# Kernel optimization log

Measured on AMD Instinct MI355X. Metric: run time of the kernel, lower is better.

Reference implementation:

```python
import jax, jax.numpy as jnp
import numpy as np

N_EXPERTS = 8
TOP_K = 2
LB_COEF = 0.01
D_MODEL = 1024
D_FF = 4096


def setup_inputs() -> dict:
    key = jax.random.key(0)
    k_x, k_r, k_w1, k_w2, k_w3 = jax.random.split(key, 5)
    x = jax.random.normal(k_x, (2, 1024, D_MODEL), dtype=jnp.float32)
    # nn.Linear(d_model, n_experts, bias=False).weight has shape (E, d_model)
    router_w = jax.random.normal(k_r, (N_EXPERTS, D_MODEL), dtype=jnp.float32) * 0.02
    # stacked expert weights; stored pre-transposed for x @ W contractions
    w1 = jax.random.normal(k_w1, (N_EXPERTS, D_MODEL, D_FF), dtype=jnp.float32) * 0.02
    w3 = jax.random.normal(k_w3, (N_EXPERTS, D_MODEL, D_FF), dtype=jnp.float32) * 0.02
    w2 = jax.random.normal(k_w2, (N_EXPERTS, D_FF, D_MODEL), dtype=jnp.float32) * 0.02
    return {"x": x, "router_w": router_w, "w1": w1, "w3": w3, "w2": w2}


def reference(x, router_w, w1, w3, w2):
    B, T, C = x.shape
    xf = x.reshape(-1, C)                      # (N, C), N = B*T
    N = xf.shape[0]

    router_logits = xf @ router_w.T            # (N, E)
    top_v, top_i = jax.lax.top_k(router_logits, TOP_K)
    top_p = jax.nn.softmax(top_v, axis=-1)     # (N, K)

    # combine weight per (token, expert): sum of top-k probs routed to expert e
    comb = jnp.zeros((N, N_EXPERTS), dtype=xf.dtype)
    comb = comb.at[jnp.arange(N)[:, None], top_i].add(top_p)  # (N, E)

    # grouped SwiGLU FFN across all experts (dense-equivalent of masked loop;
    # tokens with zero combine weight contribute nothing)
    gate = jax.nn.silu(jnp.einsum("tc,ecf->etf", xf, w1))     # (E, N, F)
    up = jnp.einsum("tc,ecf->etf", xf, w3)                    # (E, N, F)
    expert_out = jnp.einsum("etf,efc->etc", gate * up, w2)    # (E, N, C)
    out = jnp.einsum("etc,te->tc", expert_out, comb)          # (N, C)

    router_probs = jax.nn.softmax(router_logits, axis=-1)
    expert_probs = router_probs.mean(axis=0)                  # (E,)
    aux_loss = LB_COEF * N_EXPERTS * jnp.sum(expert_probs * expert_probs)

    return out.reshape(B, T, C), aux_loss
```

## Files before the change

kernel.cpp:

```cpp
#include <hip/hip_runtime.h>
#include <hip/hip_bf16.h>
#include <hip/hip_fp16.h>

#define NTOK 2048
#define DM   1024
#define DF   4096
#define NE   8
#define NROWS (NTOK * 2)
#define NSPLIT 4
#define KSPL (DF / NSPLIT)
#define FFN1_NG (32 * 16 * 8)

typedef _Float16 f16x8 __attribute__((ext_vector_type(8)));
typedef float    f32x4 __attribute__((ext_vector_type(4)));
typedef unsigned u32x2 __attribute__((ext_vector_type(2)));

__device__ __forceinline__ void gload_lds16(const void* g, void* l) {
    __builtin_amdgcn_global_load_lds(
        (const __attribute__((address_space(1))) void*)g,
        (__attribute__((address_space(3))) void*)l, 16, 0, 0);
}

__device__ __forceinline__ u32x2 pack4(float4 v) {
    _Float16 a = (_Float16)v.x, b = (_Float16)v.y,
             c = (_Float16)v.z, d = (_Float16)v.w;
    unsigned ua = __builtin_bit_cast(unsigned short, a);
    unsigned ub = __builtin_bit_cast(unsigned short, b);
    unsigned uc = __builtin_bit_cast(unsigned short, c);
    unsigned ud = __builtin_bit_cast(unsigned short, d);
    u32x2 r;
    r[0] = ua | (ub << 16);
    r[1] = uc | (ud << 16);
    return r;
}

__global__ void k_init(int* counts, float* probs_sum) {
    int i = threadIdx.x;
    if (i < NE) { counts[i] = 0; probs_sum[i] = 0.f; }
}

__device__ __forceinline__ void transpose_tile(
    float* tile ,
    const float* __restrict__ src, _Float16* __restrict__ dst,
    int K, int N, int k0, int n0, int tid)
{
    int tk = tid >> 4, tn = (tid & 15) << 2;
#pragma unroll
    for (int r = 0; r < 4; r++) {
        float4 v = *(const float4*)(src + (size_t)(k0 + tk + (r << 4)) * N + n0 + tn);
        float* trow = &tile[(tk + (r << 4)) * 65 + tn];
        trow[0] = v.x; trow[1] = v.y; trow[2] = v.z; trow[3] = v.w;
    }
    __syncthreads();
    int on = tid >> 2, ok = (tid & 3) << 4;
    unsigned pk[8];
#pragma unroll
    for (int p2 = 0; p2 < 8; p2++) {
        _Float16 a = (_Float16)tile[(ok + 2 * p2) * 65 + on];
        _Float16 b = (_Float16)tile[(ok + 2 * p2 + 1) * 65 + on];
        pk[p2] = (unsigned)(*(unsigned short*)&a) | ((unsigned)(*(unsigned short*)&b) << 16);
    }
    _Float16* d = dst + (size_t)(n0 + on) * K + k0 + ok;
    *(uint4*)d       = make_uint4(pk[0], pk[1], pk[2], pk[3]);
    *(uint4*)(d + 8) = make_uint4(pk[4], pk[5], pk[6], pk[7]);
}

__global__ __launch_bounds__(256) void k_pre(
    const float* __restrict__ x, const float* __restrict__ rw,
    const float* __restrict__ w1, const float* __restrict__ w3,
    _Float16* __restrict__ WA, _Float16* __restrict__ WB,
    int* counts, float* probs_sum,
    int* pair_exp, int* pair_pos, float* topp)
{
    __shared__ float smem[64 * 65];
    int bid = blockIdx.x;
    int tid = threadIdx.x;

    if (bid >= 128) {
        int t = bid - 128;
        int z = t >> 10, xy = t & 1023;
        int e = z & 7;
        const float* src = ((z < 8) ? w1 : w3) + (size_t)e * DM * DF;
        _Float16* dst = ((z < 8) ? WA : WB) + (size_t)e * DF * DM;
        transpose_tile(smem, src, dst, DM, DF, (xy >> 6) << 6, (xy & 63) << 6, tid);
        return;
    }

    float* lprobs = smem;
    int* lcount = (int*)(smem + 8);
    int* lbase  = (int*)(smem + 16);
    if (tid < NE) { lprobs[tid] = 0.f; lcount[tid] = 0; }
    __syncthreads();

    int l16 = tid & 15;
    int t = bid * 16 + (tid >> 4);

    const float* xt = x + (size_t)t * DM;
    float acc[NE];
#pragma unroll
    for (int e = 0; e < NE; e++) acc[e] = 0.f;

#pragma unroll
    for (int i0 = 0; i0 < DM; i0 += 64) {
        int i = i0 + l16 * 4;
        float4 xv = *(const float4*)(xt + i);
#pragma unroll
        for (int e = 0; e < NE; e++) {
            float4 wv = *(const float4*)(rw + e * DM + i);
            acc[e] = fmaf(xv.x, wv.x, acc[e]);
            acc[e] = fmaf(xv.y, wv.y, acc[e]);
            acc[e] = fmaf(xv.z, wv.z, acc[e]);
            acc[e] = fmaf(xv.w, wv.w, acc[e]);
        }
    }
#pragma unroll
    for (int m = 1; m < 16; m <<= 1)
#pragma unroll
        for (int e = 0; e < NE; e++)
            acc[e] += __shfl_xor(acc[e], m);

    int i0e = 0, i1e = 0, r0 = 0, r1 = 0;
    if (l16 == 0) {
        float mx = acc[0];
#pragma unroll
        for (int e = 1; e < NE; e++) mx = fmaxf(mx, acc[e]);
        float p[NE]; float s = 0.f;
#pragma unroll
        for (int e = 0; e < NE; e++) { p[e] = expf(acc[e] - mx); s += p[e]; }
        float inv = 1.f / s;
#pragma unroll
        for (int e = 0; e < NE; e++) atomicAdd(&lprobs[e], p[e] * inv);

        i0e = 0;
#pragma unroll
        for (int e = 1; e < NE; e++) if (acc[e] > acc[i0e]) i0e = e;
        i1e = (i0e == 0) ? 1 : 0;
#pragma unroll
        for (int e = 0; e < NE; e++) if (e != i0e && acc[e] > acc[i1e]) i1e = e;

        float e1 = expf(acc[i1e] - acc[i0e]);
        float den = 1.f / (1.f + e1);
        topp[t * 2 + 0] = den;
        topp[t * 2 + 1] = e1 * den;
        pair_exp[t * 2 + 0] = i0e;
        pair_exp[t * 2 + 1] = i1e;
        r0 = atomicAdd(&lcount[i0e], 1);
        r1 = atomicAdd(&lcount[i1e], 1);
    }
    __syncthreads();
    if (tid < NE) {
        lbase[tid] = atomicAdd(&counts[tid], lcount[tid]);
        atomicAdd(&probs_sum[tid], lprobs[tid]);
    }
    __syncthreads();
    if (l16 == 0) {
        pair_pos[t * 2 + 0] = lbase[i0e] + r0;
        pair_pos[t * 2 + 1] = lbase[i1e] + r1;
    }
}

__global__ void k_offsets(const int* counts, const float* probs_sum,
                          int* eoff, float* out_aux)
{
    if (threadIdx.x == 0 && blockIdx.x == 0) {
        int off = 0;
        for (int e = 0; e < NE; e++) { eoff[e] = off; off += counts[e]; }
        eoff[NE] = off;
        float aux = 0.f;
        for (int e = 0; e < NE; e++) {
            float ep = probs_sum[e] / (float)NTOK;
            aux += ep * ep;
        }
        out_aux[0] = 0.01f * (float)NE * aux;
    }
}

__global__ __launch_bounds__(256) void k_gather(
    const float* __restrict__ x, const int* __restrict__ pair_exp,
    const int* __restrict__ pair_pos, const int* __restrict__ eoff,
    _Float16* __restrict__ Xg)
{
    int b = blockIdx.x;
    int t = b >> 1, s = b & 1;
    int e = pair_exp[t * 2 + s];
    int row = eoff[e] + pair_pos[t * 2 + s];
    int c = threadIdx.x << 2;
    float4 v = *(const float4*)(x + (size_t)t * DM + c);
    u32x2 o = pack4(v);
    *(u32x2*)(Xg + (size_t)row * DM + c) = o;
}

__global__ __launch_bounds__(256) void k_transpose(
    const float* __restrict__ W, _Float16* __restrict__ Wt, int K, int N)
{
    __shared__ float tile[64 * 65];
    int e = blockIdx.z;
    transpose_tile(tile, W + (size_t)e * K * N, Wt + (size_t)e * N * K,
                   K, N, blockIdx.y << 6, blockIdx.x << 6, threadIdx.x);
}

__global__ __launch_bounds__(256, 2) void k_ffn1(
    const _Float16* __restrict__ A, const _Float16* __restrict__ B1t,
    const _Float16* __restrict__ B3t, _Float16* __restrict__ H,
    const int* __restrict__ counts, const int* __restrict__ eoff,
    const float* __restrict__ w2, _Float16* __restrict__ W2T)
{
    __shared__ __align__(16) unsigned char smem[49152];
    int bid = blockIdx.x;
    int tid = threadIdx.x;

    if (bid >= FFN1_NG) {
        int t = bid - FFN1_NG;
        int e = t >> 10, xy = t & 1023;
        transpose_tile((float*)smem, w2 + (size_t)e * DF * DM,
                       W2T + (size_t)e * DM * DF,
                       DF, DM, (xy >> 4) << 6, (xy & 15) << 6, tid);
        return;
    }

    int e = bid >> 9;
    int m0 = ((bid >> 5) & 15) << 7;
    int n0 = (bid & 31) << 7;
    int cnt = counts[e];
    if (m0 >= cnt) return;
    int rb = eoff[e];

    int lane = tid & 63, w = tid >> 6;
    int wr = (w >> 1) << 6, wc = (w & 1) << 6;
    int l15 = lane & 15, l4 = lane >> 4;

    const _Float16* Ab  = A   + (size_t)(rb + m0) * DM;
    const _Float16* B1b = B1t + ((size_t)e * DF + n0) * DM;
    const _Float16* B3b = B3t + ((size_t)e * DF + n0) * DM;

    int c0 = tid, c1 = tid + 256;
    int r0c = c0 >> 2, s0c = (c0 & 3) ^ ((r0c >> 1) & 3);
    int r1c = c1 >> 2, s1c = (c1 & 3) ^ ((r1c >> 1) & 3);
    size_t g0 = (size_t)r0c * DM + (s0c << 3);
    size_t g1 = (size_t)r1c * DM + (s1c << 3);

    f32x4 accg[4][4], accu[4][4];
#pragma unroll
    for (int i = 0; i < 4; i++)
#pragma unroll
        for (int j = 0; j < 4; j++) {
            accg[i][j] = (f32x4){0.f, 0.f, 0.f, 0.f};
            accu[i][j] = (f32x4){0.f, 0.f, 0.f, 0.f};
        }

    auto STAGE = [&](unsigned char* buf, int k0) {
        gload_lds16(Ab  + g0 + k0, buf + (c0 << 4));
        gload_lds16(Ab  + g1 + k0, buf + (c1 << 4));
        gload_lds16(B1b + g0 + k0, buf + 8192 + (c0 << 4));
        gload_lds16(B1b + g1 + k0, buf + 8192 + (c1 << 4));
        gload_lds16(B3b + g0 + k0, buf + 16384 + (c0 << 4));
        gload_lds16(B3b + g1 + k0, buf + 16384 + (c1 << 4));
    };
    auto COMPUTE = [&](const unsigned char* buf) {
        f16x8 af[4], b1f[4], b3f[4];
#pragma unroll
        for (int i = 0; i < 4; i++) {
            int r = wr + (i << 4) + l15;
            int s = l4 ^ ((r >> 1) & 3);
            af[i] = *(const f16x8*)(buf + (r << 6) + (s << 4));
        }
#pragma unroll
        for (int j = 0; j < 4; j++) {
            int r = wc + (j << 4) + l15;
            int s = l4 ^ ((r >> 1) & 3);
            int o = (r << 6) + (s << 4);
            b1f[j] = *(const f16x8*)(buf + 8192 + o);
            b3f[j] = *(const f16x8*)(buf + 16384 + o);
        }
        __builtin_amdgcn_s_setprio(1);
#pragma unroll
        for (int i = 0; i < 4; i++)
#pragma unroll
            for (int j = 0; j < 4; j++) {
                accg[i][j] = __builtin_amdgcn_mfma_f32_16x16x32_f16(af[i], b1f[j], accg[i][j], 0, 0, 0);
                accu[i][j] = __builtin_amdgcn_mfma_f32_16x16x32_f16(af[i], b3f[j], accu[i][j], 0, 0, 0);
            }
        __builtin_amdgcn_s_setprio(0);
    };

    unsigned char* cur = smem;
    unsigned char* nxt = smem + 24576;

    STAGE(cur, 0);
    for (int k = 32; k < DM; k += 32) {
        STAGE(nxt, k);
        __builtin_amdgcn_sched_barrier(0);
        asm volatile("s_waitcnt vmcnt(6)" ::: "memory");
        __builtin_amdgcn_s_barrier();
        __builtin_amdgcn_sched_barrier(0);
        COMPUTE(cur);
        __builtin_amdgcn_sched_barrier(0);
        __builtin_amdgcn_s_barrier();
        unsigned char* tp = cur; cur = nxt; nxt = tp;
    }
    asm volatile("s_waitcnt vmcnt(0)" ::: "memory");
    __builtin_amdgcn_s_barrier();
    __builtin_amdgcn_sched_barrier(0);
    COMPUTE(cur);

#pragma unroll
    for (int i = 0; i < 4; i++) {
#pragma unroll
        for (int rr = 0; rr < 4; rr++) {
            int m = m0 + wr + (i << 4) + (l4 << 2) + rr;
            if (m < cnt) {
                size_t go = (size_t)(rb + m) * DF + n0 + wc + l15;
#pragma unroll
                for (int j = 0; j < 4; j++) {
                    float g = accg[i][j][rr];
                    float u = accu[i][j][rr];
                    float h = g / (1.f + __expf(-g)) * u;
                    H[go + (size_t)(j << 4)] = (_Float16)h;
                }
            }
        }
    }
}

__global__ __launch_bounds__(256, 3) void k_gemm2(
    const _Float16* __restrict__ A, const _Float16* __restrict__ Bt,
    float* __restrict__ Yp,
    const int* __restrict__ counts, const int* __restrict__ eoff)
{
    __shared__ __align__(16) unsigned char smem[32768];
    int z = blockIdx.z;
    int e = z >> 2, sp = z & 3;
    int cnt = counts[e];
    int m0 = blockIdx.y << 7;
    if (m0 >= cnt) return;
    int n0 = blockIdx.x << 7;
    int rb = eoff[e];

    int tid = threadIdx.x;
    int lane = tid & 63, w = tid >> 6;
    int wr = (w >> 1) << 6, wc = (w & 1) << 6;
    int l15 = lane & 15, l4 = lane >> 4;

    const _Float16* Ab = A + (size_t)(rb + m0) * DF;
    const _Float16* Bb = Bt + ((size_t)e * DM + n0) * DF;

    int c0 = tid, c1 = tid + 256;
    int r0c = c0 >> 2, s0c = (c0 & 3) ^ ((r0c >> 1) & 3);
    int r1c = c1 >> 2, s1c = (c1 & 3) ^ ((r1c >> 1) & 3);
    size_t g0 = (size_t)r0c * DF + (s0c << 3);
    size_t g1 = (size_t)r1c * DF + (s1c << 3);

    f32x4 acc[4][4];
#pragma unroll
    for (int i = 0; i < 4; i++)
#pragma unroll
        for (int j = 0; j < 4; j++) acc[i][j] = (f32x4){0.f, 0.f, 0.f, 0.f};

    auto STAGE = [&](unsigned char* buf, int k0) {
        gload_lds16(Ab + g0 + k0, buf + (c0 << 4));
        gload_lds16(Ab + g1 + k0, buf + (c1 << 4));
        gload_lds16(Bb + g0 + k0, buf + 8192 + (c0 << 4));
        gload_lds16(Bb + g1 + k0, buf + 8192 + (c1 << 4));
    };
    auto COMPUTE = [&](const unsigned char* buf) {
        f16x8 af[4], bfr[4];
#pragma unroll
        for (int i = 0; i < 4; i++) {
            int r = wr + (i << 4) + l15;
            int s = l4 ^ ((r >> 1) & 3);
            af[i] = *(const f16x8*)(buf + (r << 6) + (s << 4));
        }
#pragma unroll
        for (int j = 0; j < 4; j++) {
            int r = wc + (j << 4) + l15;
            int s = l4 ^ ((r >> 1) & 3);
            bfr[j] = *(const f16x8*)(buf + 8192 + (r << 6) + (s << 4));
        }
        __builtin_amdgcn_s_setprio(1);
#pragma unroll
        for (int i = 0; i < 4; i++)
#pragma unroll
            for (int j = 0; j < 4; j++)
                acc[i][j] = __builtin_amdgcn_mfma_f32_16x16x32_f16(af[i], bfr[j], acc[i][j], 0, 0, 0);
        __builtin_amdgcn_s_setprio(0);
    };

    unsigned char* cur = smem;
    unsigned char* nxt = smem + 16384;
    int kbase = sp * KSPL;

    STAGE(cur, kbase);
    for (int k = 32; k < KSPL; k += 32) {
        STAGE(nxt, kbase + k);
        __builtin_amdgcn_sched_barrier(0);
        asm volatile("s_waitcnt vmcnt(4)" ::: "memory");
        __builtin_amdgcn_s_barrier();
        __builtin_amdgcn_sched_barrier(0);
        COMPUTE(cur);
        __builtin_amdgcn_sched_barrier(0);
        __builtin_amdgcn_s_barrier();
        unsigned char* tp = cur; cur = nxt; nxt = tp;
    }
    asm volatile("s_waitcnt vmcnt(0)" ::: "memory");
    __builtin_amdgcn_s_barrier();
    __builtin_amdgcn_sched_barrier(0);
    COMPUTE(cur);

    float* Yo = Yp + (size_t)sp * NROWS * DM;
#pragma unroll
    for (int i = 0; i < 4; i++) {
#pragma unroll
        for (int rr = 0; rr < 4; rr++) {
            int m = m0 + wr + (i << 4) + (l4 << 2) + rr;
            if (m < cnt) {
                size_t go = (size_t)(rb + m) * DM + n0 + wc + l15;
#pragma unroll
                for (int j = 0; j < 4; j++)
                    Yo[go + (size_t)(j << 4)] = acc[i][j][rr];
            }
        }
    }
}

__global__ __launch_bounds__(256) void k_combine(
    const float* __restrict__ Yp,
    const int* __restrict__ pair_exp, const int* __restrict__ pair_pos,
    const float* __restrict__ topp, const int* __restrict__ eoff,
    float* __restrict__ out)
{
    int t = blockIdx.x;
    int c4 = threadIdx.x * 4;
    int e0 = pair_exp[t * 2], e1 = pair_exp[t * 2 + 1];
    size_t r0 = (size_t)(eoff[e0] + pair_pos[t * 2]);
    size_t r1 = (size_t)(eoff[e1] + pair_pos[t * 2 + 1]);
    float p0 = topp[t * 2], p1 = topp[t * 2 + 1];

    float4 a = make_float4(0.f, 0.f, 0.f, 0.f);
    float4 b = make_float4(0.f, 0.f, 0.f, 0.f);
#pragma unroll
    for (int sp = 0; sp < NSPLIT; sp++) {
        const float* base = Yp + (size_t)sp * NROWS * DM;
        float4 va = *(const float4*)&base[r0 * DM + c4];
        float4 vb = *(const float4*)&base[r1 * DM + c4];
        a.x += va.x; a.y += va.y; a.z += va.z; a.w += va.w;
        b.x += vb.x; b.y += vb.y; b.z += vb.z; b.w += vb.w;
    }
    float4 o;
    o.x = p0 * a.x + p1 * b.x;
    o.y = p0 * a.y + p1 * b.y;
    o.z = p0 * a.z + p1 * b.z;
    o.w = p0 * a.w + p1 * b.w;
    *(float4*)&out[(size_t)t * DM + c4] = o;
}

extern "C" void kernel_launch(void* const* d_in, const int* in_sizes, int n_in,
                              void* d_out, int out_size, void* d_ws, size_t ws_size,
                              hipStream_t stream)
{
    const float* x  = (const float*)d_in[0];
    const float* rw = (const float*)d_in[1];
    const float* w1 = (const float*)d_in[2];
    const float* w3 = (const float*)d_in[3];
    const float* w2 = (const float*)d_in[4];
    float* out = (float*)d_out;

    char* ws = (char*)d_ws;
    int*   counts    = (int*)ws;
    float* probs_sum = (float*)(ws + 64);
    int*   eoff      = (int*)(ws + 128);
    int*   pair_exp  = (int*)(ws + 256);
    int*   pair_pos  = (int*)(ws + 256 + NROWS * 4);
    float* topp      = (float*)(ws + 256 + 2 * NROWS * 4);

    _Float16* Xg  = (_Float16*)(ws + ((size_t)1 << 20));
    _Float16* H   = (_Float16*)(ws + ((size_t)9 << 20));
    _Float16* WA  = (_Float16*)(ws + ((size_t)41 << 20));
    _Float16* WB  = (_Float16*)(ws + ((size_t)105 << 20));
    float*    Yp  = (float*)WB;
    _Float16* W2T = (_Float16*)(ws + ((size_t)169 << 20));

    bool fused = ws_size >= ((size_t)234 << 20);

    k_init<<<1, 64, 0, stream>>>(counts, probs_sum);
    k_pre<<<128 + 16384, 256, 0, stream>>>(x, rw, w1, w3, WA, WB,
                                           counts, probs_sum, pair_exp, pair_pos, topp);
    k_offsets<<<1, 1, 0, stream>>>(counts, probs_sum, eoff, out + (size_t)NTOK * DM);
    k_gather<<<NROWS, 256, 0, stream>>>(x, pair_exp, pair_pos, eoff, Xg);

    if (fused) {
        k_ffn1<<<FFN1_NG + 8192, 256, 0, stream>>>(Xg, WA, WB, H, counts, eoff, w2, W2T);
        k_gemm2<<<dim3(DM / 128, 16, NE * NSPLIT), 256, 0, stream>>>(H, W2T, Yp, counts, eoff);
    } else {
        k_ffn1<<<FFN1_NG, 256, 0, stream>>>(Xg, WA, WB, H, counts, eoff, w2, nullptr);
        k_transpose<<<dim3(DM / 64, DF / 64, NE), 256, 0, stream>>>(w2, WA, DF, DM);
        k_gemm2<<<dim3(DM / 128, 16, NE * NSPLIT), 256, 0, stream>>>(H, WA, Yp, counts, eoff);
    }

    k_combine<<<NTOK, 256, 0, stream>>>(Yp, pair_exp, pair_pos, topp, eoff, out);
}
```

Measured before the change: 292.6 us.

## Fuse expert combine into gemm2 epilogue with atomics and drop split-K

Removes the 4-way K split in the second expert GEMM and the separate combine kernel. Each gemm2 tile now scales its results by the routing probability and atomically adds them into the output row of the owning token, using per-row token/prob maps written by the gather kernel. The output is zeroed with a memset first. This removes the partial-sum buffer traffic and a launch, but cuts the gemm2 grid by four with longer K loops and adds float atomics, which also makes summation order nondeterministic.

```diff
diff --git a/kernel.cpp b/kernel.cpp
--- a/kernel.cpp
+++ b/kernel.cpp
@@ -7,8 +7,6 @@
 #define DF   4096
 #define NE   8
 #define NROWS (NTOK * 2)
-#define NSPLIT 4
-#define KSPL (DF / NSPLIT)
 #define FFN1_NG (32 * 16 * 8)
 
 typedef _Float16 f16x8 __attribute__((ext_vector_type(8)));
@@ -178,12 +176,17 @@
 __global__ __launch_bounds__(256) void k_gather(
     const float* __restrict__ x, const int* __restrict__ pair_exp,
     const int* __restrict__ pair_pos, const int* __restrict__ eoff,
-    _Float16* __restrict__ Xg)
+    const float* __restrict__ topp,
+    _Float16* __restrict__ Xg, int* __restrict__ trow, float* __restrict__ prow)
 {
     int b = blockIdx.x;
     int t = b >> 1, s = b & 1;
     int e = pair_exp[t * 2 + s];
     int row = eoff[e] + pair_pos[t * 2 + s];
+    if (threadIdx.x == 0) {
+        trow[row] = t;
+        prow[row] = topp[t * 2 + s];
+    }
     int c = threadIdx.x << 2;
     float4 v = *(const float4*)(x + (size_t)t * DM + c);
     u32x2 o = pack4(v);
@@ -324,12 +327,12 @@
 
 __global__ __launch_bounds__(256, 3) void k_gemm2(
     const _Float16* __restrict__ A, const _Float16* __restrict__ Bt,
-    float* __restrict__ Yp,
-    const int* __restrict__ counts, const int* __restrict__ eoff)
+    float* __restrict__ out,
+    const int* __restrict__ counts, const int* __restrict__ eoff,
+    const int* __restrict__ trow, const float* __restrict__ prow)
 {
     __shared__ __align__(16) unsigned char smem[32768];
-    int z = blockIdx.z;
-    int e = z >> 2, sp = z & 3;
+    int e = blockIdx.z;
     int cnt = counts[e];
     int m0 = blockIdx.y << 7;
     if (m0 >= cnt) return;
@@ -387,11 +390,10 @@
 
     unsigned char* cur = smem;
     unsigned char* nxt = smem + 16384;
-    int kbase = sp * KSPL;
-
-    STAGE(cur, kbase);
-    for (int k = 32; k < KSPL; k += 32) {
-        STAGE(nxt, kbase + k);
+
+    STAGE(cur, 0);
+    for (int k = 32; k < DF; k += 32) {
+        STAGE(nxt, k);
         __builtin_amdgcn_sched_barrier(0);
         asm volatile("s_waitcnt vmcnt(4)" ::: "memory");
         __builtin_amdgcn_s_barrier();
@@ -406,51 +408,22 @@
     __builtin_amdgcn_sched_barrier(0);
     COMPUTE(cur);
 
-    float* Yo = Yp + (size_t)sp * NROWS * DM;
 #pragma unroll
     for (int i = 0; i < 4; i++) {
 #pragma unroll
         for (int rr = 0; rr < 4; rr++) {
             int m = m0 + wr + (i << 4) + (l4 << 2) + rr;
             if (m < cnt) {
-                size_t go = (size_t)(rb + m) * DM + n0 + wc + l15;
+                int grow = rb + m;
+                int t = trow[grow];
+                float pr = prow[grow];
+                float* op = out + (size_t)t * DM + n0 + wc + l15;
 #pragma unroll
                 for (int j = 0; j < 4; j++)
-                    Yo[go + (size_t)(j << 4)] = acc[i][j][rr];
+                    atomicAdd(op + (j << 4), pr * acc[i][j][rr]);
             }
         }
     }
-}
-
-__global__ __launch_bounds__(256) void k_combine(
-    const float* __restrict__ Yp,
-    const int* __restrict__ pair_exp, const int* __restrict__ pair_pos,
-    const float* __restrict__ topp, const int* __restrict__ eoff,
-    float* __restrict__ out)
-{
-    int t = blockIdx.x;
-    int c4 = threadIdx.x * 4;
-    int e0 = pair_exp[t * 2], e1 = pair_exp[t * 2 + 1];
-    size_t r0 = (size_t)(eoff[e0] + pair_pos[t * 2]);
-    size_t r1 = (size_t)(eoff[e1] + pair_pos[t * 2 + 1]);
-    float p0 = topp[t * 2], p1 = topp[t * 2 + 1];
-
-    float4 a = make_float4(0.f, 0.f, 0.f, 0.f);
-    float4 b = make_float4(0.f, 0.f, 0.f, 0.f);
-#pragma unroll
-    for (int sp = 0; sp < NSPLIT; sp++) {
-        const float* base = Yp + (size_t)sp * NROWS * DM;
-        float4 va = *(const float4*)&base[r0 * DM + c4];
-        float4 vb = *(const float4*)&base[r1 * DM + c4];
-        a.x += va.x; a.y += va.y; a.z += va.z; a.w += va.w;
-        b.x += vb.x; b.y += vb.y; b.z += vb.z; b.w += vb.w;
-    }
-    float4 o;
-    o.x = p0 * a.x + p1 * b.x;
-    o.y = p0 * a.y + p1 * b.y;
-    o.z = p0 * a.z + p1 * b.z;
-    o.w = p0 * a.w + p1 * b.w;
-    *(float4*)&out[(size_t)t * DM + c4] = o;
 }
 
 extern "C" void kernel_launch(void* const* d_in, const int* in_sizes, int n_in,
@@ -471,30 +444,31 @@
     int*   pair_exp  = (int*)(ws + 256);
     int*   pair_pos  = (int*)(ws + 256 + NROWS * 4);
     float* topp      = (float*)(ws + 256 + 2 * NROWS * 4);
+    int*   trow      = (int*)(ws + 256 + 3 * NROWS * 4);
+    float* prow      = (float*)(ws + 256 + 4 * NROWS * 4);
 
     _Float16* Xg  = (_Float16*)(ws + ((size_t)1 << 20));
     _Float16* H   = (_Float16*)(ws + ((size_t)9 << 20));
     _Float16* WA  = (_Float16*)(ws + ((size_t)41 << 20));
     _Float16* WB  = (_Float16*)(ws + ((size_t)105 << 20));
-    float*    Yp  = (float*)WB;
     _Float16* W2T = (_Float16*)(ws + ((size_t)169 << 20));
 
     bool fused = ws_size >= ((size_t)234 << 20);
+
+    hipMemsetAsync(out, 0, (size_t)NTOK * DM * sizeof(float), stream);
 
     k_init<<<1, 64, 0, stream>>>(counts, probs_sum);
     k_pre<<<128 + 16384, 256, 0, stream>>>(x, rw, w1, w3, WA, WB,
                                            counts, probs_sum, pair_exp, pair_pos, topp);
     k_offsets<<<1, 1, 0, stream>>>(counts, probs_sum, eoff, out + (size_t)NTOK * DM);
-    k_gather<<<NROWS, 256, 0, stream>>>(x, pair_exp, pair_pos, eoff, Xg);
+    k_gather<<<NROWS, 256, 0, stream>>>(x, pair_exp, pair_pos, eoff, topp, Xg, trow, prow);
 
     if (fused) {
         k_ffn1<<<FFN1_NG + 8192, 256, 0, stream>>>(Xg, WA, WB, H, counts, eoff, w2, W2T);
-        k_gemm2<<<dim3(DM / 128, 16, NE * NSPLIT), 256, 0, stream>>>(H, W2T, Yp, counts, eoff);
+        k_gemm2<<<dim3(DM / 128, 16, NE), 256, 0, stream>>>(H, W2T, out, counts, eoff, trow, prow);
     } else {
         k_ffn1<<<FFN1_NG, 256, 0, stream>>>(Xg, WA, WB, H, counts, eoff, w2, nullptr);
         k_transpose<<<dim3(DM / 64, DF / 64, NE), 256, 0, stream>>>(w2, WA, DF, DM);
-        k_gemm2<<<dim3(DM / 128, 16, NE * NSPLIT), 256, 0, stream>>>(H, WA, Yp, counts, eoff);
-    }
-
-    k_combine<<<NTOK, 256, 0, stream>>>(Yp, pair_exp, pair_pos, topp, eoff, out);
-}
+        k_gemm2<<<dim3(DM / 128, 16, NE), 256, 0, stream>>>(H, WA, out, counts, eoff, trow, prow);
+    }
+}
```

Measured after the change: 371.3 us. 26.9% more time.

## Store split-K partials in fp16 and swizzle gemm2 block order

Applied to the files above, without the earlier changes.

The second GEMM now writes its split-K partial outputs as fp16 instead of fp32, and the combine kernel reads fp16 partials and accumulates them in fp32. This halves the partial-buffer write and read traffic. Separately, the gemm2 block index is remapped with a flat swizzle so consecutive workgroups land on different experts/splits, changing cache and scheduling locality. Rounding partials to fp16 adds precision loss before the reduction.

```diff
diff --git a/kernel.cpp b/kernel.cpp
--- a/kernel.cpp
+++ b/kernel.cpp
@@ -12,6 +12,7 @@
 #define FFN1_NG (32 * 16 * 8)
 
 typedef _Float16 f16x8 __attribute__((ext_vector_type(8)));
+typedef _Float16 f16x4 __attribute__((ext_vector_type(4)));
 typedef float    f32x4 __attribute__((ext_vector_type(4)));
 typedef unsigned u32x2 __attribute__((ext_vector_type(2)));
 
@@ -324,16 +325,20 @@
 
 __global__ __launch_bounds__(256, 3) void k_gemm2(
     const _Float16* __restrict__ A, const _Float16* __restrict__ Bt,
-    float* __restrict__ Yp,
+    _Float16* __restrict__ Yp,
     const int* __restrict__ counts, const int* __restrict__ eoff)
 {
     __shared__ __align__(16) unsigned char smem[32768];
-    int z = blockIdx.z;
-    int e = z >> 2, sp = z & 3;
+
+    int flat = blockIdx.x + (blockIdx.y << 3) + (blockIdx.z << 7);
+    int swz = ((flat & 7) << 9) + (flat >> 3);
+    int bx = swz & 7, by = (swz >> 3) & 15, bz = swz >> 7;
+
+    int e = bz >> 2, sp = bz & 3;
     int cnt = counts[e];
-    int m0 = blockIdx.y << 7;
+    int m0 = by << 7;
     if (m0 >= cnt) return;
-    int n0 = blockIdx.x << 7;
+    int n0 = bx << 7;
     int rb = eoff[e];
 
     int tid = threadIdx.x;
@@ -406,7 +411,7 @@
     __builtin_amdgcn_sched_barrier(0);
     COMPUTE(cur);
 
-    float* Yo = Yp + (size_t)sp * NROWS * DM;
+    _Float16* Yo = Yp + (size_t)sp * NROWS * DM;
 #pragma unroll
     for (int i = 0; i < 4; i++) {
 #pragma unroll
@@ -416,14 +421,14 @@
                 size_t go = (size_t)(rb + m) * DM + n0 + wc + l15;
 #pragma unroll
                 for (int j = 0; j < 4; j++)
-                    Yo[go + (size_t)(j << 4)] = acc[i][j][rr];
+                    Yo[go + (size_t)(j << 4)] = (_Float16)acc[i][j][rr];
             }
         }
     }
 }
 
 __global__ __launch_bounds__(256) void k_combine(
-    const float* __restrict__ Yp,
+    const _Float16* __restrict__ Yp,
     const int* __restrict__ pair_exp, const int* __restrict__ pair_pos,
     const float* __restrict__ topp, const int* __restrict__ eoff,
     float* __restrict__ out)
@@ -439,11 +444,11 @@
     float4 b = make_float4(0.f, 0.f, 0.f, 0.f);
 #pragma unroll
     for (int sp = 0; sp < NSPLIT; sp++) {
-        const float* base = Yp + (size_t)sp * NROWS * DM;
-        float4 va = *(const float4*)&base[r0 * DM + c4];
-        float4 vb = *(const float4*)&base[r1 * DM + c4];
-        a.x += va.x; a.y += va.y; a.z += va.z; a.w += va.w;
-        b.x += vb.x; b.y += vb.y; b.z += vb.z; b.w += vb.w;
+        const _Float16* base = Yp + (size_t)sp * NROWS * DM;
+        f16x4 va = *(const f16x4*)&base[r0 * DM + c4];
+        f16x4 vb = *(const f16x4*)&base[r1 * DM + c4];
+        a.x += (float)va[0]; a.y += (float)va[1]; a.z += (float)va[2]; a.w += (float)va[3];
+        b.x += (float)vb[0]; b.y += (float)vb[1]; b.z += (float)vb[2]; b.w += (float)vb[3];
     }
     float4 o;
     o.x = p0 * a.x + p1 * b.x;
@@ -476,7 +481,7 @@
     _Float16* H   = (_Float16*)(ws + ((size_t)9 << 20));
     _Float16* WA  = (_Float16*)(ws + ((size_t)41 << 20));
     _Float16* WB  = (_Float16*)(ws + ((size_t)105 << 20));
-    float*    Yp  = (float*)WB;
+    _Float16* Yp  = WB;
     _Float16* W2T = (_Float16*)(ws + ((size_t)169 << 20));
 
     bool fused = ws_size >= ((size_t)234 << 20);
```

New measurement: 267.6 us, median of 2. 1.09x faster.
